# Kernel optimization log

Measured on AMD Instinct MI355X. Metric: run time of the kernel, lower is better.

Reference implementation:

```python
import jax, jax.numpy as jnp
import numpy as np

B, N = 8192, 32
ND, ED, GD = 16, 8, 8
HN, HE, HG, HC = 128, 128, 128, 64
TEMP = 1.0


def setup_inputs() -> dict:
    key = jax.random.key(0)
    ks = jax.random.split(key, 16)
    def w(k, i, o):
        return jax.random.normal(k, (i, o), dtype=jnp.float32) * (1.0 / np.sqrt(i))
    inp = {
        "global_features": jax.random.normal(ks[0], (B, GD), dtype=jnp.float32),
        "node_features": jax.random.normal(ks[1], (B, N, ND), dtype=jnp.float32),
        "edge_features": jax.random.normal(ks[2], (B, N - 1, ED), dtype=jnp.float32),
        "node_mask": jax.random.randint(ks[3], (B, N), 0, 2).astype(jnp.bool_),
        # node_update MLP: in = ND + 2*ED + GD -> HN
        "Wn": w(ks[4], ND + 2 * ED + GD, HN), "bn": jnp.zeros((HN,), jnp.float32),
        # edge_update MLP: in = ED + 2*HN + GD -> HE
        "We": w(ks[5], ED + 2 * HN + GD, HE), "be": jnp.zeros((HE,), jnp.float32),
        # edge aggregation score: HE -> 1
        "Ws": w(ks[6], HE, 1), "bs": jnp.zeros((1,), jnp.float32),
        # global_update MLP: HE -> HG
        "Wg": w(ks[7], HE, HG), "bg": jnp.zeros((HG,), jnp.float32),
        # global_classifier: HG -> HC -> 1
        "Wc1": w(ks[8], HG, HC), "bc1": jnp.zeros((HC,), jnp.float32),
        "Wc2": w(ks[9], HC, 1), "bc2": jnp.zeros((1,), jnp.float32),
    }
    return inp


def reference(global_features, node_features, edge_features, node_mask,
              Wn, bn, We, be, Ws, bs, Wg, bg, Wc1, bc1, Wc2, bc2):
    f32 = jnp.float32
    # edge i connects node i and i+1 (chain graph)
    edge_mask = (node_mask[:, :-1] & node_mask[:, 1:]).astype(f32)  # [B, N-1]
    ef_masked = edge_features * edge_mask[..., None]                # [B, N-1, ED]
    # shifted gathers: edge_forward[:, :-1] = masked edges, edge_backward[:, 1:] = masked edges
    edge_forward = jnp.pad(ef_masked, ((0, 0), (0, 1), (0, 0)))     # [B, N, ED]
    edge_backward = jnp.pad(ef_masked, ((0, 0), (1, 0), (0, 0)))    # [B, N, ED]
    g = global_features  # [B, GD]
    n = node_features.shape[1]
    g_node = jnp.broadcast_to(g[:, None, :], (g.shape[0], n, g.shape[1]))
    node_input = jnp.concatenate([node_features, edge_backward, edge_forward, g_node], axis=-1)
    h_node = jax.nn.relu(node_input @ Wn + bn)                      # [B, N, HN]
    g_edge = jnp.broadcast_to(g[:, None, :], (g.shape[0], n - 1, g.shape[1]))
    edge_input = jnp.concatenate([edge_features, h_node[:, :-1], h_node[:, 1:], g_edge], axis=-1)
    h_edge = jax.nn.relu(edge_input @ We + be)                      # [B, N-1, HE]
    # masked softmax edge pooling
    scores = (h_edge @ Ws + bs)[..., 0]                             # [B, N-1]
    scores = scores * edge_mask + (1.0 - edge_mask) * -1e9
    weights = jax.nn.softmax(scores / TEMP, axis=1)[..., None]      # [B, N-1, 1]
    edge_agg = jnp.sum(h_edge * weights, axis=1)                    # [B, HE]
    h_glob = jax.nn.relu(edge_agg @ Wg + bg)                        # [B, HG]
    h_cls = jax.nn.relu(h_glob @ Wc1 + bc1)                         # [B, HC]
    y = (h_cls @ Wc2 + bc2)[..., 0]                                 # [B]
    return y
```

## Files before the change

### kernel.cpp

```cpp
#include <hip/hip_runtime.h>
#include <hip/hip_bf16.h>

#define N_  32
#define ND_ 16
#define ED_ 8
#define GD_ 8
#define HN_ 128
#define HE_ 128
#define HG_ 128
#define HC_ 64

typedef __attribute__((ext_vector_type(8))) short short8_t;
typedef __attribute__((ext_vector_type(4))) short short4_t;
typedef __attribute__((ext_vector_type(4))) float f32x4;

#define MFMA16(a, b, c) __builtin_amdgcn_mfma_f32_16x16x32_bf16((a), (b), (c), 0, 0, 0)

__device__ __forceinline__ unsigned short f2bf(float f) {
    unsigned int u = __float_as_uint(f);
    unsigned int r = u + 0x7FFFu + ((u >> 16) & 1u);
    return (unsigned short)(r >> 16);
}
__device__ __forceinline__ float bf2f(unsigned short h) {
    return __uint_as_float(((unsigned int)h) << 16);
}

#define WNS_HI 0
#define WNS_LO 4096
#define WES_HI 8192
#define WES_LO (8192 + 36864)
#define WS_USHORTS (8192 + 2 * 36864)
#define WS_BYTES (WS_USHORTS * 2)

__global__ void prep_weights(const float* __restrict__ Wn,
                             const float* __restrict__ We,
                             unsigned short* __restrict__ wsp) {
    int gid = blockIdx.x * 256 + threadIdx.x;
    if (gid >= 512 + 4608) return;
    float vals[8];
    unsigned short* dh;
    unsigned short* dl;
    if (gid < 512) {
        int l = gid & 63, n = (gid >> 6) & 7;
        int c = 16 * n + (l & 15);
#pragma unroll
        for (int i = 0; i < 8; ++i) {
            int k = 8 * (l >> 4) + i;
            vals[i] = Wn[k * HN_ + c];
        }
        dh = wsp + WNS_HI + gid * 8;
        dl = wsp + WNS_LO + gid * 8;
    } else {
        int g2 = gid - 512;
        int l = g2 & 63, n = (g2 >> 6) & 7, s = g2 >> 9;
        int c = 16 * n + (l & 15);
#pragma unroll
        for (int i = 0; i < 8; ++i) {
            int kl = 8 * (l >> 4) + i;
            int ks;
            if (s <= 4) {
                int kf = s * 32 + kl;
                ks = (kf < 128) ? (8 + kf) : ((kf < 136) ? (kf - 128) : -1);
            } else {
                ks = 136 + (s - 5) * 32 + kl;
            }
            vals[i] = (ks >= 0) ? We[ks * HE_ + c] : 0.0f;
        }
        dh = wsp + WES_HI + g2 * 8;
        dl = wsp + WES_LO + g2 * 8;
    }
    unsigned short h[8], lo[8];
#pragma unroll
    for (int i = 0; i < 8; ++i) {
        h[i] = f2bf(vals[i]);
        lo[i] = f2bf(vals[i] - bf2f(h[i]));
    }
    *(short8_t*)dh = *(short8_t*)h;
    *(short8_t*)dl = *(short8_t*)lo;
}

#define HNS 168
#define NIS 40
#define HES 128

#define LOADB(Bv, ss) do {                                                      \
    Bv[0] = *(const short8_t*)(wsp + WES_HI + ((ss)*8 + 2*w)     * 512 + l*8);  \
    Bv[1] = *(const short8_t*)(wsp + WES_HI + ((ss)*8 + 2*w + 1) * 512 + l*8);  \
    Bv[2] = *(const short8_t*)(wsp + WES_LO + ((ss)*8 + 2*w)     * 512 + l*8);  \
    Bv[3] = *(const short8_t*)(wsp + WES_LO + ((ss)*8 + 2*w + 1) * 512 + l*8);  \
} while (0)

__global__ __launch_bounds__(256, 4) void gnn_mfma12(
    const float* __restrict__ gf, const float* __restrict__ nf,
    const float* __restrict__ ef, const void* __restrict__ nmask_raw,
    const float* __restrict__ Wn, const float* __restrict__ bn,
    const float* __restrict__ We, const float* __restrict__ be,
    const float* __restrict__ Ws, const float* __restrict__ bs,
    const float* __restrict__ Wg, const float* __restrict__ bg,
    const float* __restrict__ Wc1, const float* __restrict__ bc1,
    const float* __restrict__ Wc2, const float* __restrict__ bc2,
    const unsigned short* __restrict__ wsp,
    float* __restrict__ out, int Btot)
{
    const int b = blockIdx.x;
    const int t = threadIdx.x;
    const int gid0 = 2 * b;
    const int gid1 = (2 * b + 1 < Btot) ? (2 * b + 1) : (Btot - 1);

    __shared__ __align__(16) unsigned char UNI[32768];
    __shared__ __align__(16) unsigned char U3[4096];
    __shared__ __align__(16) float s_bias1[2][HN_];
    __shared__ __align__(16) float s_bias2[2][HE_];
    __shared__ float s_g[2][GD_];
    __shared__ int   s_mi[2][N_];
    __shared__ float s_emask[2][N_];
    __shared__ float s_sc[2][N_];
    __shared__ float s_w[2][N_];

#define HNG(g, row) ((unsigned short*)(UNI + (g) * 11088) + (row) * HNS)
    unsigned short* ninH = (unsigned short*)(UNI + 22176);
#define NINR(r) (ninH + (r) * NIS)
    float* heF  = (float*)UNI;
    float* efrF = (float*)U3;
    float* tmpF = (float*)U3;
    float* aggf = (float*)(U3 + 2048);
    float* hgF  = (float*)(U3 + 3072);

    const unsigned char* mb = (const unsigned char*)nmask_raw;
    int cnt = __syncthreads_count(mb[t] != 0);
    const bool is_u8 = (cnt > 96);

    if (t < 16) s_g[t >> 3][t & 7] = gf[(t >> 3 ? gid1 : gid0) * GD_ + (t & 7)];
    {
        int idx4 = t * 4;
        int gg = idx4 >> 9, rem = idx4 & 511;
        float4 v = *(const float4*)(nf + (gg ? gid1 : gid0) * 512 + rem);
        unsigned short hv[4] = {f2bf(v.x), f2bf(v.y), f2bf(v.z), f2bf(v.w)};
        *(short4_t*)&NINR(gg * 32 + (rem >> 4))[rem & 15] = *(short4_t*)hv;
    }
#pragma unroll
    for (int ii = 0; ii < 2; ++ii) {
        int idx = t + ii * 256;
        int gg = idx >> 8, rem = idx & 255, e = rem >> 3, k = rem & 7;
        efrF[(gg * 32 + e) * 8 + k] =
            (e < 31) ? ef[(gg ? gid1 : gid0) * 248 + e * 8 + k] : 0.0f;
    }
    if (t < 16) {
        int gg = t >> 3, k = t & 7;
        NINR(gg * 32)[16 + k] = 0;
    }
    for (int idx = t; idx < 2 * HNS; idx += 256) {
        int g = idx >= HNS, c = idx - g * HNS;
        HNG(g, N_)[c] = 0;
    }
    for (int idx = t; idx < 2 * 32 * 24; idx += 256) {
        int g = idx >= 768, r2 = idx - g * 768;
        int rr = r2 / 24, cc = 136 + (r2 % 24);
        HNG(g, rr)[cc] = 0;
    }
    if (t < 64) {
        int g = t >> 5, n = t & 31;
        int mv = is_u8 ? (int)mb[(g ? gid1 : gid0) * N_ + n]
                       : ((const int*)nmask_raw)[(g ? gid1 : gid0) * N_ + n];
        s_mi[g][n] = mv;
    }
    __syncthreads();

    if (t < 64) {
        int g = t >> 5, n = t & 31;
        s_emask[g][n] = (n < 31 && s_mi[g][n] != 0 && s_mi[g][n + 1] != 0) ? 1.0f : 0.0f;
    }
    {
        int mat = t >> 7, j = t & 127;
        const float* Wt = mat ? (We + (ED_ + 2 * HN_) * HE_) : (Wn + (ND_ + 2 * ED_) * HN_);
        float base = mat ? be[j] : bn[j];
        float a0 = base, a1 = base;
#pragma unroll
        for (int k = 0; k < GD_; ++k) {
            float wv = Wt[k * 128 + j];
            a0 += s_g[0][k] * wv;
            a1 += s_g[1][k] * wv;
        }
        if (mat) { s_bias2[0][j] = a0; s_bias2[1][j] = a1; }
        else     { s_bias1[0][j] = a0; s_bias1[1][j] = a1; }
    }
    __syncthreads();

#pragma unroll
    for (int ii = 0; ii < 2; ++ii) {
        int idx = t + ii * 256;
        int gg = idx >> 8, rem = idx & 255, e = rem >> 3, k = rem & 7;
        int r = gg * 32 + e;
        float vr = efrF[r * 8 + k];
        HNG(gg, e)[128 + k] = f2bf(vr);
        bool m = (e < 31) && s_mi[gg][e] != 0 && s_mi[gg][e + 1] != 0;
        unsigned short hm = f2bf(m ? vr : 0.0f);
        if (e < 31) NINR(r + 1)[16 + k] = hm;
        NINR(r)[24 + k] = hm;
    }
    __syncthreads();

    const int w = t >> 6, l = t & 63;
    const int lrow = l & 15;
    const int lk8 = (l >> 4) * 8;
    const int g4 = (l >> 4) * 4;
    const int c0 = 32 * w + lrow, c1 = c0 + 16;

    {
        const unsigned short* pn = wsp + (2 * w) * 512 + l * 8;
        short8_t nBh0 = *(const short8_t*)(pn + WNS_HI);
        short8_t nBl0 = *(const short8_t*)(pn + WNS_LO);
        short8_t nBh1 = *(const short8_t*)(pn + WNS_HI + 512);
        short8_t nBl1 = *(const short8_t*)(pn + WNS_LO + 512);

        f32x4 acc[4][2];
#pragma unroll
        for (int mt = 0; mt < 4; ++mt) {
            int g = mt >> 1;
            float b0 = s_bias1[g][c0], b1 = s_bias1[g][c1];
            acc[mt][0] = (f32x4){b0, b0, b0, b0};
            acc[mt][1] = (f32x4){b1, b1, b1, b1};
        }
#pragma unroll
        for (int mt = 0; mt < 4; ++mt) {
            int r = (mt >> 1) * 32 + (mt & 1) * 16 + lrow;
            short8_t A = *(const short8_t*)&NINR(r)[lk8];
            acc[mt][0] = MFMA16(A, nBl0, acc[mt][0]);
            acc[mt][0] = MFMA16(A, nBh0, acc[mt][0]);
            acc[mt][1] = MFMA16(A, nBl1, acc[mt][1]);
            acc[mt][1] = MFMA16(A, nBh1, acc[mt][1]);
        }
#pragma unroll
        for (int mt = 0; mt < 4; ++mt) {
            int g = mt >> 1, rb = (mt & 1) * 16 + g4;
#pragma unroll
            for (int nt = 0; nt < 2; ++nt) {
                int col = nt ? c1 : c0;
#pragma unroll
                for (int r = 0; r < 4; ++r)
                    HNG(g, rb + r)[col] = f2bf(fmaxf(acc[mt][nt][r], 0.0f));
            }
        }
    }
    __syncthreads();

    {
        f32x4 acc[4][2];
#pragma unroll
        for (int mt = 0; mt < 4; ++mt) {
            int g = mt >> 1;
            float b0 = s_bias2[g][c0], b1 = s_bias2[g][c1];
            acc[mt][0] = (f32x4){b0, b0, b0, b0};
            acc[mt][1] = (f32x4){b1, b1, b1, b1};
        }
        short8_t B1[4], B2[4];
        LOADB(B1, 0);
#pragma unroll
        for (int s = 0; s < 4; ++s) {
            LOADB(B2, 5 + s);
            int kb = s * 32 + lk8;
#pragma unroll
            for (int mt = 0; mt < 4; ++mt) {
                int g = mt >> 1, lr = (mt & 1) * 16 + lrow;
                short8_t A1 = *(const short8_t*)&HNG(g, lr)[kb];
                acc[mt][0] = MFMA16(A1, B1[2], acc[mt][0]);
                acc[mt][0] = MFMA16(A1, B1[0], acc[mt][0]);
                acc[mt][1] = MFMA16(A1, B1[3], acc[mt][1]);
                acc[mt][1] = MFMA16(A1, B1[1], acc[mt][1]);
            }
            LOADB(B1, s + 1);
#pragma unroll
            for (int mt = 0; mt < 4; ++mt) {
                int g = mt >> 1, lr = (mt & 1) * 16 + lrow;
                short8_t A2 = *(const short8_t*)&HNG(g, lr + 1)[kb];
                acc[mt][0] = MFMA16(A2, B2[2], acc[mt][0]);
                acc[mt][0] = MFMA16(A2, B2[0], acc[mt][0]);
                acc[mt][1] = MFMA16(A2, B2[3], acc[mt][1]);
                acc[mt][1] = MFMA16(A2, B2[1], acc[mt][1]);
            }
        }
        {
            int kb = 128 + lk8;
#pragma unroll
            for (int mt = 0; mt < 4; ++mt) {
                int g = mt >> 1, lr = (mt & 1) * 16 + lrow;
                short8_t A1 = *(const short8_t*)&HNG(g, lr)[kb];
                acc[mt][0] = MFMA16(A1, B1[2], acc[mt][0]);
                acc[mt][0] = MFMA16(A1, B1[0], acc[mt][0]);
                acc[mt][1] = MFMA16(A1, B1[3], acc[mt][1]);
                acc[mt][1] = MFMA16(A1, B1[1], acc[mt][1]);
            }
        }
        __syncthreads();
#pragma unroll
        for (int mt = 0; mt < 4; ++mt) {
            int g = mt >> 1, rb = (mt & 1) * 16 + g4;
#pragma unroll
            for (int nt = 0; nt < 2; ++nt) {
                int col = nt ? c1 : c0;
#pragma unroll
                for (int r = 0; r < 4; ++r)
                    heF[(g * 32 + rb + r) * HES + col] = fmaxf(acc[mt][nt][r], 0.0f);
            }
        }
    }
    __syncthreads();

    {
        int c = t & 3, eg = t >> 2;
        int g = eg >> 5, e = eg & 31;
        const float* he = &heF[(g * 32 + e) * HES];
        float pq = 0.0f;
#pragma unroll
        for (int j0 = 0; j0 < 32; j0 += 4) {
            float4 h = *(const float4*)&he[c * 32 + j0];
            float4 wv = *(const float4*)&Ws[c * 32 + j0];
            pq += h.x * wv.x + h.y * wv.y + h.z * wv.z + h.w * wv.w;
        }
        pq += __shfl_xor(pq, 1);
        pq += __shfl_xor(pq, 2);
        if (c == 0) s_sc[g][e] = pq + bs[0];
    }
    __syncthreads();

    if (t < 128) {
        int g = t >> 6, tt = t & 63;
        float v = -INFINITY;
        if (tt < 31)
            v = s_sc[g][tt] * s_emask[g][tt] + (1.0f - s_emask[g][tt]) * (-1e9f);
        float m = v;
#pragma unroll
        for (int d = 32; d >= 1; d >>= 1) m = fmaxf(m, __shfl_xor(m, d));
        float e_ = (tt < 31) ? expf(v - m) : 0.0f;
        float ssum = e_;
#pragma unroll
        for (int d = 32; d >= 1; d >>= 1) ssum += __shfl_xor(ssum, d);
        if (tt < 32) s_w[g][tt] = (tt < 31) ? (e_ / ssum) : 0.0f;
    }
    __syncthreads();

    {
        int g = t >> 7, j = t & 127;
        float pp = 0.0f;
#pragma unroll
        for (int e = 0; e < 31; ++e)
            pp += heF[(g * 32 + e) * HES + j] * s_w[g][e];
        aggf[g * 128 + j] = pp;
    }
    __syncthreads();

    {
        int j = t & 127, half = t >> 7;
        float a0 = 0.0f, a1 = 0.0f;
        for (int k = half * 64; k < half * 64 + 64; ++k) {
            float wv = Wg[k * HG_ + j];
            a0 += aggf[k] * wv;
            a1 += aggf[128 + k] * wv;
        }
        tmpF[half * 256 + j] = a0;
        tmpF[half * 256 + 128 + j] = a1;
    }
    __syncthreads();
    {
        int g = t >> 7, j = t & 127;
        hgF[g * 128 + j] = fmaxf(tmpF[g * 128 + j] + tmpF[256 + g * 128 + j] + bg[j], 0.0f);
    }
    __syncthreads();

    {
        int j = t & 63, q = t >> 6;
        float a0 = 0.0f, a1 = 0.0f;
        for (int k = q * 32; k < q * 32 + 32; ++k) {
            float wv = Wc1[k * HC_ + j];
            a0 += hgF[k] * wv;
            a1 += hgF[128 + k] * wv;
        }
        tmpF[q * 128 + j] = a0;
        tmpF[q * 128 + 64 + j] = a1;
    }
    __syncthreads();
    if (t < 128) {
        int g = t >> 6, tt = t & 63;
        float hc = bc1[tt];
#pragma unroll
        for (int q = 0; q < 4; ++q) hc += tmpF[q * 128 + g * 64 + tt];
        hc = fmaxf(hc, 0.0f);
        float pp = hc * Wc2[tt];
#pragma unroll
        for (int d = 32; d >= 1; d >>= 1) pp += __shfl_xor(pp, d);
        if (tt == 0 && 2 * b + g < Btot) out[2 * b + g] = pp + bc2[0];
    }
#undef HNG
#undef NINR
}

__device__ __forceinline__ void tile_fma_4x4(
    float acc[4][4], const float* in0, const float* in1, const float* in2,
    const float* in3, int k, const float* __restrict__ W, int wrow, int c4)
{
    float in_[4][4];
    *(float4*)&in_[0][0] = *(const float4*)(in0 + k);
    *(float4*)&in_[1][0] = *(const float4*)(in1 + k);
    *(float4*)&in_[2][0] = *(const float4*)(in2 + k);
    *(float4*)&in_[3][0] = *(const float4*)(in3 + k);
#pragma unroll
    for (int kk = 0; kk < 4; ++kk) {
        float w_[4];
        *(float4*)w_ = *(const float4*)&W[(wrow + kk) * 128 + c4];
#pragma unroll
        for (int r = 0; r < 4; ++r)
#pragma unroll
            for (int c = 0; c < 4; ++c)
                acc[r][c] += in_[r][kk] * w_[c];
    }
}

__global__ __launch_bounds__(256, 3) void gnn_fused(
    const float* __restrict__ gf, const float* __restrict__ nf,
    const float* __restrict__ ef, const void* __restrict__ nmask_raw,
    const float* __restrict__ Wn, const float* __restrict__ bn,
    const float* __restrict__ We, const float* __restrict__ be,
    const float* __restrict__ Ws, const float* __restrict__ bs,
    const float* __restrict__ Wg, const float* __restrict__ bg,
    const float* __restrict__ Wc1, const float* __restrict__ bc1,
    const float* __restrict__ Wc2, const float* __restrict__ bc2,
    float* __restrict__ out)
{
    const int b = blockIdx.x;
    const int t = threadIdx.x;

    __shared__ __align__(16) float s_g[GD_];
    __shared__ int   s_mi[N_];
    __shared__ float s_emask[N_];
    __shared__ __align__(16) float s_ef[N_][ED_];
    __shared__ __align__(16) float s_efm[N_][ED_];
    __shared__ __align__(16) float s_nin[N_][32];
    __shared__ __align__(16) float s_hn[N_ + 1][HN_];
    __shared__ __align__(16) float s_he[N_][HE_];
    __shared__ __align__(16) float s_bias1[HN_];
    __shared__ __align__(16) float s_bias2[HE_];
    __shared__ float s_sc[N_];
    __shared__ float s_w[N_];
    __shared__ __align__(16) float s_tmp[256];
    __shared__ __align__(16) float s_aggf[HE_];
    __shared__ __align__(16) float s_hg[HG_];
    __shared__ __align__(16) float s_hc[HC_];

    const unsigned char* mb = (const unsigned char*)nmask_raw;
    int cnt = __syncthreads_count(mb[t] != 0);
    const bool is_u8 = (cnt > 96);

    if (t < GD_) s_g[t] = gf[b * GD_ + t];
    for (int idx = t; idx < N_ * ND_; idx += 256)
        s_nin[idx >> 4][idx & 15] = nf[b * N_ * ND_ + idx];
    for (int idx = t; idx < (N_ - 1) * ED_; idx += 256)
        s_ef[idx >> 3][idx & 7] = ef[b * (N_ - 1) * ED_ + idx];
    if (t < ED_) s_ef[N_ - 1][t] = 0.0f;
    if (t < HN_) s_hn[N_][t] = 0.0f;
    if (t < N_) {
        int mv = is_u8 ? (int)mb[b * N_ + t] : ((const int*)nmask_raw)[b * N_ + t];
        s_mi[t] = mv;
    }
    __syncthreads();

    if (t < N_)
        s_emask[t] = (t < N_ - 1 && s_mi[t] != 0 && s_mi[t + 1] != 0) ? 1.0f : 0.0f;
    __syncthreads();

    {
        int e = t >> 3, k = t & 7;
        s_efm[e][k] = s_ef[e][k] * s_emask[e];
    }
    {
        int j = t & 127;
        if (t < 128) {
            float v = bn[j];
#pragma unroll
            for (int k = 0; k < GD_; ++k)
                v += s_g[k] * Wn[(ND_ + 2 * ED_ + k) * HN_ + j];
            s_bias1[j] = v;
        } else {
            float v = be[j];
#pragma unroll
            for (int k = 0; k < GD_; ++k)
                v += s_g[k] * We[(ED_ + 2 * HN_ + k) * HE_ + j];
            s_bias2[j] = v;
        }
    }
    __syncthreads();

    for (int idx = t; idx < N_ * 16; idx += 256) {
        int n = idx >> 4, kk = idx & 15;
        if (kk < 8) s_nin[n][16 + kk]       = (n > 0)      ? s_efm[n - 1][kk] : 0.0f;
        else        s_nin[n][24 + (kk - 8)] = (n < N_ - 1) ? s_efm[n][kk - 8] : 0.0f;
    }
    __syncthreads();

    const int jg = t & 31, rg = t >> 5;
    const int c4 = jg * 4, r4 = rg * 4;

    {
        float acc[4][4];
#pragma unroll
        for (int r = 0; r < 4; ++r)
#pragma unroll
            for (int c = 0; c < 4; ++c) acc[r][c] = s_bias1[c4 + c];
        const float* i0 = &s_nin[r4 + 0][0];
        const float* i1 = &s_nin[r4 + 1][0];
        const float* i2 = &s_nin[r4 + 2][0];
        const float* i3 = &s_nin[r4 + 3][0];
#pragma unroll
        for (int k = 0; k < 32; k += 4)
            tile_fma_4x4(acc, i0, i1, i2, i3, k, Wn, k, c4);
#pragma unroll
        for (int r = 0; r < 4; ++r)
#pragma unroll
            for (int c = 0; c < 4; ++c)
                s_hn[r4 + r][c4 + c] = fmaxf(acc[r][c], 0.0f);
    }
    __syncthreads();

    {
        float acc[4][4];
#pragma unroll
        for (int r = 0; r < 4; ++r)
#pragma unroll
            for (int c = 0; c < 4; ++c) acc[r][c] = s_bias2[c4 + c];
        {
            const float* i0 = &s_ef[r4 + 0][0];
            const float* i1 = &s_ef[r4 + 1][0];
            const float* i2 = &s_ef[r4 + 2][0];
            const float* i3 = &s_ef[r4 + 3][0];
#pragma unroll
            for (int k = 0; k < 8; k += 4)
                tile_fma_4x4(acc, i0, i1, i2, i3, k, We, k, c4);
        }
        {
            const float* i0 = &s_hn[r4 + 0][0];
            const float* i1 = &s_hn[r4 + 1][0];
            const float* i2 = &s_hn[r4 + 2][0];
            const float* i3 = &s_hn[r4 + 3][0];
#pragma unroll 4
            for (int k = 0; k < 128; k += 4)
                tile_fma_4x4(acc, i0, i1, i2, i3, k, We, 8 + k, c4);
        }
        {
            const float* i0 = &s_hn[r4 + 1][0];
            const float* i1 = &s_hn[r4 + 2][0];
            const float* i2 = &s_hn[r4 + 3][0];
            const float* i3 = &s_hn[r4 + 4][0];
#pragma unroll 4
            for (int k = 0; k < 128; k += 4)
                tile_fma_4x4(acc, i0, i1, i2, i3, k, We, 136 + k, c4);
        }
#pragma unroll
        for (int r = 0; r < 4; ++r)
#pragma unroll
            for (int c = 0; c < 4; ++c)
                s_he[r4 + r][c4 + c] = fmaxf(acc[r][c], 0.0f);
    }
    __syncthreads();

    {
        int c = t & 7, e = t >> 3;
        const float* he = &s_he[e][0];
        float p = 0.0f;
#pragma unroll
        for (int j0 = 0; j0 < 16; j0 += 4) {
            float4 h = *(const float4*)&he[c * 16 + j0];
            float4 wv = *(const float4*)&Ws[c * 16 + j0];
            p += h.x * wv.x + h.y * wv.y + h.z * wv.z + h.w * wv.w;
        }
        p += __shfl_xor(p, 1);
        p += __shfl_xor(p, 2);
        p += __shfl_xor(p, 4);
        if (c == 0) s_sc[e] = p + bs[0];
    }
    __syncthreads();
    if (t < 64) {
        float v = -INFINITY;
        if (t < N_ - 1)
            v = s_sc[t] * s_emask[t] + (1.0f - s_emask[t]) * (-1e9f);
        float m = v;
#pragma unroll
        for (int d = 32; d >= 1; d >>= 1) m = fmaxf(m, __shfl_xor(m, d));
        float e_ = (t < N_ - 1) ? expf(v - m) : 0.0f;
        float ssum = e_;
#pragma unroll
        for (int d = 32; d >= 1; d >>= 1) ssum += __shfl_xor(ssum, d);
        if (t < N_) s_w[t] = (t < N_ - 1) ? (e_ / ssum) : 0.0f;
    }
    __syncthreads();

    {
        int j = t & 127, half = t >> 7;
        float p = 0.0f;
#pragma unroll
        for (int e = 0; e < 16; ++e) {
            int ee = half * 16 + e;
            p += s_he[ee][j] * s_w[ee];
        }
        s_tmp[half * 128 + j] = p;
    }
    __syncthreads();
    if (t < 128) s_aggf[t] = s_tmp[t] + s_tmp[128 + t];
    __syncthreads();

    {
        int j = t & 127, half = t >> 7;
        float p = 0.0f;
        for (int k = half * 64; k < half * 64 + 64; ++k)
            p += s_aggf[k] * Wg[k * HG_ + j];
        s_tmp[half * 128 + j] = p;
    }
    __syncthreads();
    if (t < 128) s_hg[t] = fmaxf(s_tmp[t] + s_tmp[128 + t] + bg[t], 0.0f);
    __syncthreads();

    {
        int j = t & 63, q = t >> 6;
        float p = 0.0f;
        for (int k = q * 32; k < q * 32 + 32; ++k)
            p += s_hg[k] * Wc1[k * HC_ + j];
        s_tmp[q * 64 + j] = p;
    }
    __syncthreads();
    if (t < 64)
        s_hc[t] = fmaxf(s_tmp[t] + s_tmp[64 + t] + s_tmp[128 + t] + s_tmp[192 + t] + bc1[t], 0.0f);
    __syncthreads();

    if (t < 64) {
        float p = s_hc[t] * Wc2[t];
#pragma unroll
        for (int d = 32; d >= 1; d >>= 1) p += __shfl_xor(p, d);
        if (t == 0) out[b] = p + bc2[0];
    }
}

extern "C" void kernel_launch(void* const* d_in, const int* in_sizes, int n_in,
                              void* d_out, int out_size, void* d_ws, size_t ws_size,
                              hipStream_t stream) {
    const float* gf  = (const float*)d_in[0];
    const float* nf  = (const float*)d_in[1];
    const float* ef  = (const float*)d_in[2];
    const void*  nm  = d_in[3];
    const float* Wn  = (const float*)d_in[4];
    const float* bn  = (const float*)d_in[5];
    const float* We  = (const float*)d_in[6];
    const float* be  = (const float*)d_in[7];
    const float* Ws  = (const float*)d_in[8];
    const float* bs  = (const float*)d_in[9];
    const float* Wg  = (const float*)d_in[10];
    const float* bg  = (const float*)d_in[11];
    const float* Wc1 = (const float*)d_in[12];
    const float* bc1 = (const float*)d_in[13];
    const float* Wc2 = (const float*)d_in[14];
    const float* bc2 = (const float*)d_in[15];
    float* out = (float*)d_out;

    const int B = in_sizes[0] / GD_;

    if (ws_size >= (size_t)WS_BYTES && B >= 2) {
        prep_weights<<<20, 256, 0, stream>>>(Wn, We, (unsigned short*)d_ws);
        const int NB = (B + 1) / 2;
        gnn_mfma12<<<NB, 256, 0, stream>>>(gf, nf, ef, nm, Wn, bn, We, be, Ws, bs,
                                           Wg, bg, Wc1, bc1, Wc2, bc2,
                                           (const unsigned short*)d_ws, out, B);
    } else {
        gnn_fused<<<B, 256, 0, stream>>>(gf, nf, ef, nm, Wn, bn, We, be, Ws, bs,
                                         Wg, bg, Wc1, bc1, Wc2, bc2, out);
    }
}
```

Before: 77.70 us.

## Move global-update and classifier MLPs onto split-bf16 MFMA with prepacked weights

Adds a new kernel variant that runs the Wg and Wc1 matmuls (global update and classifier head) on MFMA, using hi/lo bf16-split weights that the prep kernel now also packs into the workspace. This replaces what were presumably scalar FP32 dot products in the tail of the per-graph kernel. The cost is a larger workspace requirement and extra prep work. It also depends on the workspace being large enough; otherwise the code falls back to the older path.

Result: slower. 79.61 us (+2.5%).

```diff
diff --git a/kernel.cpp b/kernel.cpp
--- a/kernel.cpp
+++ b/kernel.cpp
@@ -31,12 +31,20 @@
 #define WES_LO (8192 + 36864)
 #define WS_USHORTS (8192 + 2 * 36864)
 #define WS_BYTES (WS_USHORTS * 2)
+#define WGS_HI 81920
+#define WGS_LO (81920 + 16384)
+#define WC1S_HI 114688
+#define WC1S_LO (114688 + 8192)
+#define WS2_USHORTS 131072
+#define WS2_BYTES (WS2_USHORTS * 2)
 
 __global__ void prep_weights(const float* __restrict__ Wn,
                              const float* __restrict__ We,
+                             const float* __restrict__ Wg,
+                             const float* __restrict__ Wc1,
                              unsigned short* __restrict__ wsp) {
     int gid = blockIdx.x * 256 + threadIdx.x;
-    if (gid >= 512 + 4608) return;
+    if (gid >= 8192) return;
     float vals[8];
     unsigned short* dh;
     unsigned short* dl;
@@ -50,7 +58,7 @@
         }
         dh = wsp + WNS_HI + gid * 8;
         dl = wsp + WNS_LO + gid * 8;
-    } else {
+    } else if (gid < 5120) {
         int g2 = gid - 512;
         int l = g2 & 63, n = (g2 >> 6) & 7, s = g2 >> 9;
         int c = 16 * n + (l & 15);
@@ -68,6 +76,28 @@
         }
         dh = wsp + WES_HI + g2 * 8;
         dl = wsp + WES_LO + g2 * 8;
+    } else if (gid < 7168) {
+        int g3 = gid - 5120;
+        int l = g3 & 63, n = (g3 >> 6) & 7, s = g3 >> 9;
+        int c = 16 * n + (l & 15);
+#pragma unroll
+        for (int i = 0; i < 8; ++i) {
+            int k = 32 * s + 8 * (l >> 4) + i;
+            vals[i] = Wg[k * HG_ + c];
+        }
+        dh = wsp + WGS_HI + g3 * 8;
+        dl = wsp + WGS_LO + g3 * 8;
+    } else {
+        int g4 = gid - 7168;
+        int l = g4 & 63, n = (g4 >> 6) & 3, s = g4 >> 8;
+        int c = 16 * n + (l & 15);
+#pragma unroll
+        for (int i = 0; i < 8; ++i) {
+            int k = 32 * s + 8 * (l >> 4) + i;
+            vals[i] = Wc1[k * HC_ + c];
+        }
+        dh = wsp + WC1S_HI + g4 * 8;
+        dl = wsp + WC1S_LO + g4 * 8;
     }
     unsigned short h[8], lo[8];
 #pragma unroll
@@ -89,6 +119,338 @@
     Bv[2] = *(const short8_t*)(wsp + WES_LO + ((ss)*8 + 2*w)     * 512 + l*8);  \
     Bv[3] = *(const short8_t*)(wsp + WES_LO + ((ss)*8 + 2*w + 1) * 512 + l*8);  \
 } while (0)
+
+__global__ __launch_bounds__(256, 4) void gnn_mfma13(
+    const float* __restrict__ gf, const float* __restrict__ nf,
+    const float* __restrict__ ef, const void* __restrict__ nmask_raw,
+    const float* __restrict__ Wn, const float* __restrict__ bn,
+    const float* __restrict__ We, const float* __restrict__ be,
+    const float* __restrict__ Ws, const float* __restrict__ bs,
+    const float* __restrict__ Wg, const float* __restrict__ bg,
+    const float* __restrict__ Wc1, const float* __restrict__ bc1,
+    const float* __restrict__ Wc2, const float* __restrict__ bc2,
+    const unsigned short* __restrict__ wsp,
+    float* __restrict__ out, int Btot)
+{
+    const int b = blockIdx.x;
+    const int t = threadIdx.x;
+    const int gid0 = 2 * b;
+    const int gid1 = (2 * b + 1 < Btot) ? (2 * b + 1) : (Btot - 1);
+
+    __shared__ __align__(16) unsigned char UNI[32768];
+    __shared__ __align__(16) unsigned char U3[4096];
+    __shared__ __align__(16) float s_bias1[2][HN_];
+    __shared__ __align__(16) float s_bias2[2][HE_];
+    __shared__ float s_g[2][GD_];
+    __shared__ int   s_mi[2][N_];
+    __shared__ float s_emask[2][N_];
+    __shared__ float s_sc[2][N_];
+    __shared__ float s_w[2][N_];
+
+#define HNG(g, row) ((unsigned short*)(UNI + (g) * 11088) + (row) * HNS)
+    unsigned short* ninH = (unsigned short*)(UNI + 22176);
+#define NINR(r) (ninH + (r) * NIS)
+    float* heF  = (float*)UNI;
+    float* efrF = (float*)U3;
+    unsigned short* aggB = (unsigned short*)U3;
+    unsigned short* hgB  = (unsigned short*)(U3 + 512);
+    float* hcF  = (float*)(U3 + 1024);
+
+    const unsigned char* mb = (const unsigned char*)nmask_raw;
+    int cnt = __syncthreads_count(mb[t] != 0);
+    const bool is_u8 = (cnt > 96);
+
+    if (t < 16) s_g[t >> 3][t & 7] = gf[(t >> 3 ? gid1 : gid0) * GD_ + (t & 7)];
+    {
+        int idx4 = t * 4;
+        int gg = idx4 >> 9, rem = idx4 & 511;
+        float4 v = *(const float4*)(nf + (gg ? gid1 : gid0) * 512 + rem);
+        unsigned short hv[4] = {f2bf(v.x), f2bf(v.y), f2bf(v.z), f2bf(v.w)};
+        *(short4_t*)&NINR(gg * 32 + (rem >> 4))[rem & 15] = *(short4_t*)hv;
+    }
+#pragma unroll
+    for (int ii = 0; ii < 2; ++ii) {
+        int idx = t + ii * 256;
+        int gg = idx >> 8, rem = idx & 255, e = rem >> 3, k = rem & 7;
+        efrF[(gg * 32 + e) * 8 + k] =
+            (e < 31) ? ef[(gg ? gid1 : gid0) * 248 + e * 8 + k] : 0.0f;
+    }
+    if (t < 16) {
+        int gg = t >> 3, k = t & 7;
+        NINR(gg * 32)[16 + k] = 0;
+    }
+    for (int idx = t; idx < 2 * HNS; idx += 256) {
+        int g = idx >= HNS, c = idx - g * HNS;
+        HNG(g, N_)[c] = 0;
+    }
+    for (int idx = t; idx < 2 * 32 * 24; idx += 256) {
+        int g = idx >= 768, r2 = idx - g * 768;
+        int rr = r2 / 24, cc = 136 + (r2 % 24);
+        HNG(g, rr)[cc] = 0;
+    }
+    if (t < 64) {
+        int g = t >> 5, n = t & 31;
+        int mv = is_u8 ? (int)mb[(g ? gid1 : gid0) * N_ + n]
+                       : ((const int*)nmask_raw)[(g ? gid1 : gid0) * N_ + n];
+        s_mi[g][n] = mv;
+    }
+    __syncthreads();
+
+    if (t < 64) {
+        int g = t >> 5, n = t & 31;
+        s_emask[g][n] = (n < 31 && s_mi[g][n] != 0 && s_mi[g][n + 1] != 0) ? 1.0f : 0.0f;
+    }
+    {
+        int mat = t >> 7, j = t & 127;
+        const float* Wt = mat ? (We + (ED_ + 2 * HN_) * HE_) : (Wn + (ND_ + 2 * ED_) * HN_);
+        float base = mat ? be[j] : bn[j];
+        float a0 = base, a1 = base;
+#pragma unroll
+        for (int k = 0; k < GD_; ++k) {
+            float wv = Wt[k * 128 + j];
+            a0 += s_g[0][k] * wv;
+            a1 += s_g[1][k] * wv;
+        }
+        if (mat) { s_bias2[0][j] = a0; s_bias2[1][j] = a1; }
+        else     { s_bias1[0][j] = a0; s_bias1[1][j] = a1; }
+    }
+    __syncthreads();
+
+#pragma unroll
+    for (int ii = 0; ii < 2; ++ii) {
+        int idx = t + ii * 256;
+        int gg = idx >> 8, rem = idx & 255, e = rem >> 3, k = rem & 7;
+        int r = gg * 32 + e;
+        float vr = efrF[r * 8 + k];
+        HNG(gg, e)[128 + k] = f2bf(vr);
+        bool m = (e < 31) && s_mi[gg][e] != 0 && s_mi[gg][e + 1] != 0;
+        unsigned short hm = f2bf(m ? vr : 0.0f);
+        if (e < 31) NINR(r + 1)[16 + k] = hm;
+        NINR(r)[24 + k] = hm;
+    }
+    __syncthreads();
+
+    const int w = t >> 6, l = t & 63;
+    const int lrow = l & 15;
+    const int lk8 = (l >> 4) * 8;
+    const int g4 = (l >> 4) * 4;
+    const int c0 = 32 * w + lrow, c1 = c0 + 16;
+
+    {
+        const unsigned short* pn = wsp + (2 * w) * 512 + l * 8;
+        short8_t nBh0 = *(const short8_t*)(pn + WNS_HI);
+        short8_t nBl0 = *(const short8_t*)(pn + WNS_LO);
+        short8_t nBh1 = *(const short8_t*)(pn + WNS_HI + 512);
+        short8_t nBl1 = *(const short8_t*)(pn + WNS_LO + 512);
+
+        f32x4 acc[4][2];
+#pragma unroll
+        for (int mt = 0; mt < 4; ++mt) {
+            int g = mt >> 1;
+            float b0 = s_bias1[g][c0], b1 = s_bias1[g][c1];
+            acc[mt][0] = (f32x4){b0, b0, b0, b0};
+            acc[mt][1] = (f32x4){b1, b1, b1, b1};
+        }
+#pragma unroll
+        for (int mt = 0; mt < 4; ++mt) {
+            int r = (mt >> 1) * 32 + (mt & 1) * 16 + lrow;
+            short8_t A = *(const short8_t*)&NINR(r)[lk8];
+            acc[mt][0] = MFMA16(A, nBl0, acc[mt][0]);
+            acc[mt][0] = MFMA16(A, nBh0, acc[mt][0]);
+            acc[mt][1] = MFMA16(A, nBl1, acc[mt][1]);
+            acc[mt][1] = MFMA16(A, nBh1, acc[mt][1]);
+        }
+#pragma unroll
+        for (int mt = 0; mt < 4; ++mt) {
+            int g = mt >> 1, rb = (mt & 1) * 16 + g4;
+#pragma unroll
+            for (int nt = 0; nt < 2; ++nt) {
+                int col = nt ? c1 : c0;
+#pragma unroll
+                for (int r = 0; r < 4; ++r)
+                    HNG(g, rb + r)[col] = f2bf(fmaxf(acc[mt][nt][r], 0.0f));
+            }
+        }
+    }
+    __syncthreads();
+
+    {
+        f32x4 acc[4][2];
+#pragma unroll
+        for (int mt = 0; mt < 4; ++mt) {
+            int g = mt >> 1;
+            float b0 = s_bias2[g][c0], b1 = s_bias2[g][c1];
+            acc[mt][0] = (f32x4){b0, b0, b0, b0};
+            acc[mt][1] = (f32x4){b1, b1, b1, b1};
+        }
+        short8_t B1[4], B2[4];
+        LOADB(B1, 0);
+#pragma unroll
+        for (int s = 0; s < 4; ++s) {
+            LOADB(B2, 5 + s);
+            int kb = s * 32 + lk8;
+#pragma unroll
+            for (int mt = 0; mt < 4; ++mt) {
+                int g = mt >> 1, lr = (mt & 1) * 16 + lrow;
+                short8_t A1 = *(const short8_t*)&HNG(g, lr)[kb];
+                acc[mt][0] = MFMA16(A1, B1[2], acc[mt][0]);
+                acc[mt][0] = MFMA16(A1, B1[0], acc[mt][0]);
+                acc[mt][1] = MFMA16(A1, B1[3], acc[mt][1]);
+                acc[mt][1] = MFMA16(A1, B1[1], acc[mt][1]);
+            }
+            LOADB(B1, s + 1);
+#pragma unroll
+            for (int mt = 0; mt < 4; ++mt) {
+                int g = mt >> 1, lr = (mt & 1) * 16 + lrow;
+                short8_t A2 = *(const short8_t*)&HNG(g, lr + 1)[kb];
+                acc[mt][0] = MFMA16(A2, B2[2], acc[mt][0]);
+                acc[mt][0] = MFMA16(A2, B2[0], acc[mt][0]);
+                acc[mt][1] = MFMA16(A2, B2[3], acc[mt][1]);
+                acc[mt][1] = MFMA16(A2, B2[1], acc[mt][1]);
+            }
+        }
+        {
+            int kb = 128 + lk8;
+#pragma unroll
+            for (int mt = 0; mt < 4; ++mt) {
+                int g = mt >> 1, lr = (mt & 1) * 16 + lrow;
+                short8_t A1 = *(const short8_t*)&HNG(g, lr)[kb];
+                acc[mt][0] = MFMA16(A1, B1[2], acc[mt][0]);
+                acc[mt][0] = MFMA16(A1, B1[0], acc[mt][0]);
+                acc[mt][1] = MFMA16(A1, B1[3], acc[mt][1]);
+                acc[mt][1] = MFMA16(A1, B1[1], acc[mt][1]);
+            }
+        }
+        __syncthreads();
+#pragma unroll
+        for (int mt = 0; mt < 4; ++mt) {
+            int g = mt >> 1, rb = (mt & 1) * 16 + g4;
+#pragma unroll
+            for (int nt = 0; nt < 2; ++nt) {
+                int col = nt ? c1 : c0;
+#pragma unroll
+                for (int r = 0; r < 4; ++r)
+                    heF[(g * 32 + rb + r) * HES + col] = fmaxf(acc[mt][nt][r], 0.0f);
+            }
+        }
+    }
+    __syncthreads();
+
+    {
+        int c = t & 3, eg = t >> 2;
+        int g = eg >> 5, e = eg & 31;
+        const float* he = &heF[(g * 32 + e) * HES];
+        float pq = 0.0f;
+#pragma unroll
+        for (int j0 = 0; j0 < 32; j0 += 4) {
+            float4 h = *(const float4*)&he[c * 32 + j0];
+            float4 wv = *(const float4*)&Ws[c * 32 + j0];
+            pq += h.x * wv.x + h.y * wv.y + h.z * wv.z + h.w * wv.w;
+        }
+        pq += __shfl_xor(pq, 1);
+        pq += __shfl_xor(pq, 2);
+        if (c == 0) s_sc[g][e] = pq + bs[0];
+    }
+    __syncthreads();
+
+    if (t < 128) {
+        int g = t >> 6, tt = t & 63;
+        float v = -INFINITY;
+        if (tt < 31)
+            v = s_sc[g][tt] * s_emask[g][tt] + (1.0f - s_emask[g][tt]) * (-1e9f);
+        float m = v;
+#pragma unroll
+        for (int d = 32; d >= 1; d >>= 1) m = fmaxf(m, __shfl_xor(m, d));
+        float e_ = (tt < 31) ? expf(v - m) : 0.0f;
+        float ssum = e_;
+#pragma unroll
+        for (int d = 32; d >= 1; d >>= 1) ssum += __shfl_xor(ssum, d);
+        if (tt < 32) s_w[g][tt] = (tt < 31) ? (e_ / ssum) : 0.0f;
+    }
+    __syncthreads();
+
+    {
+        int g = t >> 7, j = t & 127;
+        float pp = 0.0f;
+#pragma unroll
+        for (int e = 0; e < 31; ++e)
+            pp += heF[(g * 32 + e) * HES + j] * s_w[g][e];
+        aggB[g * 128 + j] = f2bf(pp);
+    }
+    __syncthreads();
+
+    {
+        f32x4 acc5[2];
+        acc5[0] = (f32x4){0.f, 0.f, 0.f, 0.f};
+        acc5[1] = acc5[0];
+#pragma unroll
+        for (int s = 0; s < 4; ++s) {
+            unsigned short av[8] = {0, 0, 0, 0, 0, 0, 0, 0};
+            if (lrow < 2)
+                *(short8_t*)av = *(const short8_t*)&aggB[lrow * 128 + 32 * s + lk8];
+            short8_t A5 = *(short8_t*)av;
+            const unsigned short* pb = wsp + (s * 8 + 2 * w) * 512 + l * 8;
+            short8_t Bh0 = *(const short8_t*)(pb + WGS_HI);
+            short8_t Bl0 = *(const short8_t*)(pb + WGS_LO);
+            short8_t Bh1 = *(const short8_t*)(pb + WGS_HI + 512);
+            short8_t Bl1 = *(const short8_t*)(pb + WGS_LO + 512);
+            acc5[0] = MFMA16(A5, Bl0, acc5[0]);
+            acc5[0] = MFMA16(A5, Bh0, acc5[0]);
+            acc5[1] = MFMA16(A5, Bl1, acc5[1]);
+            acc5[1] = MFMA16(A5, Bh1, acc5[1]);
+        }
+        if (l < 16) {
+#pragma unroll
+            for (int nt = 0; nt < 2; ++nt) {
+                int col = 16 * (2 * w + nt) + lrow;
+                hgB[col]       = f2bf(fmaxf(acc5[nt][0] + bg[col], 0.0f));
+                hgB[128 + col] = f2bf(fmaxf(acc5[nt][1] + bg[col], 0.0f));
+            }
+        }
+    }
+    __syncthreads();
+
+    if (w < 2) {
+        f32x4 acc6[2];
+        acc6[0] = (f32x4){0.f, 0.f, 0.f, 0.f};
+        acc6[1] = acc6[0];
+#pragma unroll
+        for (int s = 0; s < 4; ++s) {
+            unsigned short av[8] = {0, 0, 0, 0, 0, 0, 0, 0};
+            if (lrow < 2)
+                *(short8_t*)av = *(const short8_t*)&hgB[lrow * 128 + 32 * s + lk8];
+            short8_t A6 = *(short8_t*)av;
+            const unsigned short* pb = wsp + (s * 4 + 2 * w) * 512 + l * 8;
+            short8_t Bh0 = *(const short8_t*)(pb + WC1S_HI);
+            short8_t Bl0 = *(const short8_t*)(pb + WC1S_LO);
+            short8_t Bh1 = *(const short8_t*)(pb + WC1S_HI + 512);
+            short8_t Bl1 = *(const short8_t*)(pb + WC1S_LO + 512);
+            acc6[0] = MFMA16(A6, Bl0, acc6[0]);
+            acc6[0] = MFMA16(A6, Bh0, acc6[0]);
+            acc6[1] = MFMA16(A6, Bl1, acc6[1]);
+            acc6[1] = MFMA16(A6, Bh1, acc6[1]);
+        }
+        if (l < 16) {
+#pragma unroll
+            for (int nt = 0; nt < 2; ++nt) {
+                int col = 16 * (2 * w + nt) + lrow;
+                hcF[col]      = fmaxf(acc6[nt][0] + bc1[col], 0.0f);
+                hcF[64 + col] = fmaxf(acc6[nt][1] + bc1[col], 0.0f);
+            }
+        }
+    }
+    __syncthreads();
+
+    if (t < 128) {
+        int g = t >> 6, tt = t & 63;
+        float pp = hcF[g * 64 + tt] * Wc2[tt];
+#pragma unroll
+        for (int d = 32; d >= 1; d >>= 1) pp += __shfl_xor(pp, d);
+        if (tt == 0 && 2 * b + g < Btot) out[2 * b + g] = pp + bc2[0];
+    }
+#undef HNG
+#undef NINR
+}
 
 __global__ __launch_bounds__(256, 4) void gnn_mfma12(
     const float* __restrict__ gf, const float* __restrict__ nf,
@@ -660,8 +1022,14 @@
 
     const int B = in_sizes[0] / GD_;
 
-    if (ws_size >= (size_t)WS_BYTES && B >= 2) {
-        prep_weights<<<20, 256, 0, stream>>>(Wn, We, (unsigned short*)d_ws);
+    if (ws_size >= (size_t)WS2_BYTES && B >= 2) {
+        prep_weights<<<32, 256, 0, stream>>>(Wn, We, Wg, Wc1, (unsigned short*)d_ws);
+        const int NB = (B + 1) / 2;
+        gnn_mfma13<<<NB, 256, 0, stream>>>(gf, nf, ef, nm, Wn, bn, We, be, Ws, bs,
+                                           Wg, bg, Wc1, bc1, Wc2, bc2,
+                                           (const unsigned short*)d_ws, out, B);
+    } else if (ws_size >= (size_t)WS_BYTES && B >= 2) {
+        prep_weights<<<20, 256, 0, stream>>>(Wn, We, Wg, Wc1, (unsigned short*)d_ws);
         const int NB = (B + 1) / 2;
         gnn_mfma12<<<NB, 256, 0, stream>>>(gf, nf, ef, nm, Wn, bn, We, be, Ws, bs,
                                            Wg, bg, Wc1, bc1, Wc2, bc2,
```
